# Kernel tuning notes

Hardware: AMD Instinct MI355X
Metric: run time of the kernel (lower is better)

Reference implementation:

```python
import jax, jax.numpy as jnp
import numpy as np

MARGIN = 0.35
EPS = 1e-12  # matches F.normalize default eps


def setup_inputs() -> dict:
    key = jax.random.key(0)
    k1, k2 = jax.random.split(key)
    B, N, D = 64, 1024, 128
    embeddings = jax.random.normal(k1, (B, N, D), dtype=jnp.float32)
    labels = jax.random.randint(k2, (B, N), 0, 2, dtype=jnp.int64)
    return {"embeddings": embeddings, "labels": labels}


def reference(embeddings, labels):
    # L2-normalize along last dim (F.normalize semantics)
    norm = jnp.linalg.norm(embeddings, axis=-1, keepdims=True)
    emb = embeddings / jnp.maximum(norm, EPS)  # [B, N, D]

    pos = (labels == 1)  # [B, N]
    neg = (labels == 0)  # [B, N]
    n_pos = pos.sum(axis=-1)  # [B]
    n_neg = neg.sum(axis=-1)  # [B]
    valid = (n_pos > 0) & (n_neg > 0)  # [B]

    # pairwise similarity: positive i vs negative j within each sample
    sim = jnp.einsum('bnd,bmd->bnm', emb, emb)  # [B, N, N]
    hinge = jax.nn.relu(sim - 0.5 + MARGIN)  # [B, N, N]

    # per-positive mean over negatives
    neg_f = neg.astype(emb.dtype)
    per_pos_sum = jnp.einsum('bnm,bm->bn', hinge, neg_f)  # sum over negatives
    denom = jnp.maximum(n_neg, 1).astype(emb.dtype)[:, None]
    per_pos_mean = per_pos_sum / denom  # [B, N]

    pos_f = pos.astype(emb.dtype)
    valid_f = valid.astype(emb.dtype)
    loss_sum = jnp.sum(per_pos_mean * pos_f * valid_f[:, None])
    count = jnp.sum(n_pos * valid)
    return loss_sum / jnp.maximum(count, 1).astype(emb.dtype)
```

## Files before the change

### kernel.cpp

```cpp
#include <hip/hip_runtime.h>
#include <stdint.h>


#define B_    64
#define N_    1024
#define D_    128
#define NPAD  640
#define T_    5

typedef __attribute__((ext_vector_type(8))) short short8;
typedef __attribute__((ext_vector_type(4))) float floatx4;
typedef __attribute__((ext_vector_type(4))) unsigned short ushortx4;

__device__ __forceinline__ unsigned short f2bf_rne(float f) {
    union { float f; unsigned u; } cv; cv.f = f;
    unsigned u = cv.u;
    return (unsigned short)((u + 0x7FFFu + ((u >> 16) & 1u)) >> 16);
}

__global__ __launch_bounds__(256) void scan_kernel(
    const long long* __restrict__ lab,
    unsigned short* __restrict__ posIdx,
    unsigned short* __restrict__ negIdx,
    int* __restrict__ npos)
{
    __shared__ int wsum[4];
    const int b = blockIdx.x, t = threadIdx.x;
    const int w = t >> 6, lane = t & 63;
    const long long* lb = lab + (size_t)b * N_;

    int l[4], c = 0;
    #pragma unroll
    for (int i = 0; i < 4; ++i) { l[i] = (int)lb[t * 4 + i]; c += l[i]; }

    int sc = c;
    #pragma unroll
    for (int off = 1; off < 64; off <<= 1) {
        int v = __shfl_up(sc, off);
        if (lane >= off) sc += v;
    }
    if (lane == 63) wsum[w] = sc;
    __syncthreads();
    int base = 0;
    for (int k = 0; k < w; ++k) base += wsum[k];

    int pe = base + sc - c;
    #pragma unroll
    for (int i = 0; i < 4; ++i) {
        const int n = t * 4 + i;
        if (l[i]) { if (pe < NPAD) posIdx[b * NPAD + pe] = (unsigned short)n; }
        else      { const int ne = n - pe; if (ne < NPAD) negIdx[b * NPAD + ne] = (unsigned short)n; }
        pe += l[i];
    }
    if (t == 255) npos[b] = base + sc;
}

__global__ __launch_bounds__(256) void prep_kernel(
    const float* __restrict__ emb,
    const unsigned short* __restrict__ posIdx,
    const unsigned short* __restrict__ negIdx,
    const int* __restrict__ npos,
    ushortx4* __restrict__ Apos_c,
    ushortx4* __restrict__ Aneg_c)
{
    const int w    = threadIdx.x >> 6;
    const int lane = threadIdx.x & 63;
    const int gw   = blockIdx.x * 4 + w;
    const int half = lane >> 5, sl = lane & 31;

    const int side = gw >= (B_ * NPAD / 2);
    const int p2   = side ? gw - (B_ * NPAD / 2) : gw;
    const int b    = p2 / (NPAD / 2);
    const int slot = (p2 % (NPAD / 2)) * 2 + half;

    const int np    = npos[b];
    const int count = side ? (N_ - np) : np;
    const unsigned short* idxArr = side ? negIdx : posIdx;

    float4 v = make_float4(0.f, 0.f, 0.f, 0.f);
    if (slot < count) {
        const int n = idxArr[b * NPAD + slot];
        v = *(const float4*)(emb + ((size_t)(b * N_ + n)) * D_ + sl * 4);
    }
    float ss = v.x * v.x + v.y * v.y + v.z * v.z + v.w * v.w;
    #pragma unroll
    for (int off = 16; off; off >>= 1) ss += __shfl_xor(ss, off);
    const float scale = 1.0f / fmaxf(sqrtf(ss), 1e-12f);

    ushortx4 o;
    o.x = f2bf_rne(v.x * scale); o.y = f2bf_rne(v.y * scale);
    o.z = f2bf_rne(v.z * scale); o.w = f2bf_rne(v.w * scale);
    ushortx4* dst = side ? Aneg_c : Apos_c;
    dst[(size_t)(b * NPAD + slot) * (D_ / 4) + sl] = o;
}

__global__ __launch_bounds__(256, 2) void gemm_hinge_kernel(
    const unsigned short* __restrict__ Apos_c,
    const unsigned short* __restrict__ Aneg_c,
    float* __restrict__ Stile)
{
    __shared__ unsigned short ldsA[128 * 128];
    __shared__ unsigned short ldsB[128 * 128];
    __shared__ float sred[4];

    const int t    = threadIdx.x;
    const int w    = t >> 6;
    const int lane = t & 63;
    const int tm = blockIdx.x, tn = blockIdx.y, b = blockIdx.z;

    const char* gA = (const char*)(Apos_c + ((size_t)b * NPAD + (size_t)tm * 128) * D_);
    const char* gB = (const char*)(Aneg_c + ((size_t)b * NPAD + (size_t)tn * 128) * D_);

    auto lA = (__attribute__((address_space(3))) char*)ldsA;
    auto lB = (__attribute__((address_space(3))) char*)ldsB;

    #pragma unroll
    for (int it = 0; it < 8; ++it) {
        const int p   = it * 4096 + t * 16;
        const int row = p >> 8;
        const int c   = (p >> 4) & 15;
        const int goff = (row << 8) | ((c ^ (row & 15)) << 4);
        __builtin_amdgcn_global_load_lds(
            (const __attribute__((address_space(1))) void*)(gA + goff),
            (__attribute__((address_space(3))) void*)(lA + it * 4096 + w * 1024),
            16, 0, 0);
        __builtin_amdgcn_global_load_lds(
            (const __attribute__((address_space(1))) void*)(gB + goff),
            (__attribute__((address_space(3))) void*)(lB + it * 4096 + w * 1024),
            16, 0, 0);
    }
    __syncthreads();

    const int wm = w & 1, wn = w >> 1;
    const int r = lane & 15, quad = lane >> 4;

    floatx4 acc[4][4] = {};
    #pragma unroll
    for (int ks = 0; ks < 4; ++ks) {
        short8 af[4], bf[4];
        const int cc = (((ks << 2) + quad) ^ r) << 3;
        #pragma unroll
        for (int i = 0; i < 4; ++i) {
            af[i] = *(const short8*)(ldsA + (wm * 64 + i * 16 + r) * 128 + cc);
            bf[i] = *(const short8*)(ldsB + (wn * 64 + i * 16 + r) * 128 + cc);
        }
        #pragma unroll
        for (int i = 0; i < 4; ++i)
            #pragma unroll
            for (int j = 0; j < 4; ++j)
                acc[i][j] = __builtin_amdgcn_mfma_f32_16x16x32_bf16(
                    af[i], bf[j], acc[i][j], 0, 0, 0);
    }

    float s = 0.f;
    #pragma unroll
    for (int i = 0; i < 4; ++i)
        #pragma unroll
        for (int j = 0; j < 4; ++j)
            #pragma unroll
            for (int k2 = 0; k2 < 4; ++k2)
                s += fmaxf(acc[i][j][k2] - 0.15f, 0.f);

    #pragma unroll
    for (int off = 32; off; off >>= 1) s += __shfl_down(s, off);
    if (lane == 0) sred[w] = s;
    __syncthreads();
    if (t == 0)
        Stile[b * (T_ * T_) + tm * T_ + tn] = sred[0] + sred[1] + sred[2] + sred[3];
}

__global__ void finalize_kernel(const float* __restrict__ Stile,
                                const int* __restrict__ npos,
                                float* __restrict__ out)
{
    const int b = threadIdx.x;
    const int np = npos[b];
    const int nn = N_ - np;
    float S = 0.f;
    #pragma unroll
    for (int k = 0; k < T_ * T_; ++k) S += Stile[b * (T_ * T_) + k];
    const bool valid = (np > 0) && (nn > 0);
    float ls = valid ? S / (float)nn : 0.f;
    float c  = valid ? (float)np : 0.f;
    #pragma unroll
    for (int off = 32; off; off >>= 1) {
        ls += __shfl_down(ls, off);
        c  += __shfl_down(c, off);
    }
    if (b == 0) out[0] = ls / fmaxf(c, 1.f);
}

extern "C" void kernel_launch(void* const* d_in, const int* in_sizes, int n_in,
                              void* d_out, int out_size, void* d_ws, size_t ws_size,
                              hipStream_t stream)
{
    const float*     emb = (const float*)d_in[0];
    const long long* lab = (const long long*)d_in[1];
    float* out = (float*)d_out;

    char* ws = (char*)d_ws;
    float* Stile = (float*)ws;
    int*   npos  = (int*)(ws + (16 << 10));
    unsigned short* posIdx = (unsigned short*)(ws + (32 << 10));
    unsigned short* negIdx = (unsigned short*)(ws + (160 << 10));
    unsigned short* Apos_c = (unsigned short*)(ws + (1 << 20));
    unsigned short* Aneg_c = Apos_c + (size_t)B_ * NPAD * D_;

    scan_kernel<<<B_, 256, 0, stream>>>(lab, posIdx, negIdx, npos);

    prep_kernel<<<B_ * NPAD / 4, 256, 0, stream>>>(
        emb, posIdx, negIdx, npos, (ushortx4*)Apos_c, (ushortx4*)Aneg_c);

    dim3 grid(T_, T_, B_);
    gemm_hinge_kernel<<<grid, 256, 0, stream>>>(Apos_c, Aneg_c, Stile);

    finalize_kernel<<<1, 64, 0, stream>>>(Stile, npos, out);
}
```

Measured before the change: 99.16 us.

## Use FP8 MFMA, skip empty tiles, and fuse finalize into GEMM via last-block ticket

Normalized embeddings are now packed to FP8 instead of BF16, and the GEMM uses the fp8 16x16x32 MFMA with a halved LDS footprint and an adjusted swizzle. Tiles that fall entirely in padding are skipped. The separate finalize kernel is removed: the last block, detected with an atomic ticket counter, performs the final reduction. FP8 precision raises the risk of accuracy drift in the hinge sum, and the atomic counter adds some serialization.

```diff
diff --git a/kernel.cpp b/kernel.cpp
--- a/kernel.cpp
+++ b/kernel.cpp
@@ -7,26 +7,23 @@
 #define D_    128
 #define NPAD  640
 #define T_    5
-
-typedef __attribute__((ext_vector_type(8))) short short8;
+#define NTILE (T_ * T_)
+#define NBLK  (T_ * T_ * B_)
+
 typedef __attribute__((ext_vector_type(4))) float floatx4;
 typedef __attribute__((ext_vector_type(4))) unsigned short ushortx4;
-
-__device__ __forceinline__ unsigned short f2bf_rne(float f) {
-    union { float f; unsigned u; } cv; cv.f = f;
-    unsigned u = cv.u;
-    return (unsigned short)((u + 0x7FFFu + ((u >> 16) & 1u)) >> 16);
-}
 
 __global__ __launch_bounds__(256) void scan_kernel(
     const long long* __restrict__ lab,
     unsigned short* __restrict__ posIdx,
     unsigned short* __restrict__ negIdx,
-    int* __restrict__ npos)
+    int* __restrict__ npos,
+    int* __restrict__ counter)
 {
     __shared__ int wsum[4];
     const int b = blockIdx.x, t = threadIdx.x;
     const int w = t >> 6, lane = t & 63;
+    if (b == 0 && t == 0) *counter = 0;
     const long long* lb = lab + (size_t)b * N_;
 
     int l[4], c = 0;
@@ -60,8 +57,8 @@
     const unsigned short* __restrict__ posIdx,
     const unsigned short* __restrict__ negIdx,
     const int* __restrict__ npos,
-    ushortx4* __restrict__ Apos_c,
-    ushortx4* __restrict__ Aneg_c)
+    unsigned int* __restrict__ Apos_c,
+    unsigned int* __restrict__ Aneg_c)
 {
     const int w    = threadIdx.x >> 6;
     const int lane = threadIdx.x & 63;
@@ -87,107 +84,125 @@
     for (int off = 16; off; off >>= 1) ss += __shfl_xor(ss, off);
     const float scale = 1.0f / fmaxf(sqrtf(ss), 1e-12f);
 
-    ushortx4 o;
-    o.x = f2bf_rne(v.x * scale); o.y = f2bf_rne(v.y * scale);
-    o.z = f2bf_rne(v.z * scale); o.w = f2bf_rne(v.w * scale);
-    ushortx4* dst = side ? Aneg_c : Apos_c;
-    dst[(size_t)(b * NPAD + slot) * (D_ / 4) + sl] = o;
-}
-
-__global__ __launch_bounds__(256, 2) void gemm_hinge_kernel(
-    const unsigned short* __restrict__ Apos_c,
-    const unsigned short* __restrict__ Aneg_c,
-    float* __restrict__ Stile)
-{
-    __shared__ unsigned short ldsA[128 * 128];
-    __shared__ unsigned short ldsB[128 * 128];
+    unsigned int pk = 0;
+    pk = __builtin_amdgcn_cvt_pk_fp8_f32(v.x * scale, v.y * scale, pk, false);
+    pk = __builtin_amdgcn_cvt_pk_fp8_f32(v.z * scale, v.w * scale, pk, true);
+
+    unsigned int* dst = side ? Aneg_c : Apos_c;
+    dst[(size_t)(b * NPAD + slot) * (D_ / 4) + sl] = pk;
+}
+
+__global__ __launch_bounds__(256, 3) void gemm_hinge_kernel(
+    const unsigned char* __restrict__ Apos_c,
+    const unsigned char* __restrict__ Aneg_c,
+    const int* __restrict__ npos,
+    float* __restrict__ Stile,
+    int* __restrict__ counter,
+    float* __restrict__ out)
+{
+    __shared__ unsigned char ldsA[128 * 128];
+    __shared__ unsigned char ldsB[128 * 128];
     __shared__ float sred[4];
+    __shared__ int lastFlag;
 
     const int t    = threadIdx.x;
     const int w    = t >> 6;
     const int lane = t & 63;
     const int tm = blockIdx.x, tn = blockIdx.y, b = blockIdx.z;
 
-    const char* gA = (const char*)(Apos_c + ((size_t)b * NPAD + (size_t)tm * 128) * D_);
-    const char* gB = (const char*)(Aneg_c + ((size_t)b * NPAD + (size_t)tn * 128) * D_);
-
-    auto lA = (__attribute__((address_space(3))) char*)ldsA;
-    auto lB = (__attribute__((address_space(3))) char*)ldsB;
-
-    #pragma unroll
-    for (int it = 0; it < 8; ++it) {
-        const int p   = it * 4096 + t * 16;
-        const int row = p >> 8;
-        const int c   = (p >> 4) & 15;
-        const int goff = (row << 8) | ((c ^ (row & 15)) << 4);
-        __builtin_amdgcn_global_load_lds(
-            (const __attribute__((address_space(1))) void*)(gA + goff),
-            (__attribute__((address_space(3))) void*)(lA + it * 4096 + w * 1024),
-            16, 0, 0);
-        __builtin_amdgcn_global_load_lds(
-            (const __attribute__((address_space(1))) void*)(gB + goff),
-            (__attribute__((address_space(3))) void*)(lB + it * 4096 + w * 1024),
-            16, 0, 0);
-    }
-    __syncthreads();
-
-    const int wm = w & 1, wn = w >> 1;
-    const int r = lane & 15, quad = lane >> 4;
-
-    floatx4 acc[4][4] = {};
-    #pragma unroll
-    for (int ks = 0; ks < 4; ++ks) {
-        short8 af[4], bf[4];
-        const int cc = (((ks << 2) + quad) ^ r) << 3;
-        #pragma unroll
-        for (int i = 0; i < 4; ++i) {
-            af[i] = *(const short8*)(ldsA + (wm * 64 + i * 16 + r) * 128 + cc);
-            bf[i] = *(const short8*)(ldsB + (wn * 64 + i * 16 + r) * 128 + cc);
+    const int np = npos[b];
+    const int nn = N_ - np;
+    const bool active = (tm * 128 < np) && (tn * 128 < nn);
+
+    float tileSum = 0.f;
+    if (active) {
+        const char* gA = (const char*)(Apos_c + ((size_t)b * NPAD + (size_t)tm * 128) * D_);
+        const char* gB = (const char*)(Aneg_c + ((size_t)b * NPAD + (size_t)tn * 128) * D_);
+        auto lA = (__attribute__((address_space(3))) char*)ldsA;
+        auto lB = (__attribute__((address_space(3))) char*)ldsB;
+
+        #pragma unroll
+        for (int it = 0; it < 4; ++it) {
+            const int p   = it * 4096 + t * 16;
+            const int row = p >> 7;
+            const int c   = (p >> 4) & 7;
+            const int goff = (row << 7) | ((c ^ (row & 7)) << 4);
+            __builtin_amdgcn_global_load_lds(
+                (const __attribute__((address_space(1))) void*)(gA + goff),
+                (__attribute__((address_space(3))) void*)(lA + it * 4096 + w * 1024),
+                16, 0, 0);
+            __builtin_amdgcn_global_load_lds(
+                (const __attribute__((address_space(1))) void*)(gB + goff),
+                (__attribute__((address_space(3))) void*)(lB + it * 4096 + w * 1024),
+                16, 0, 0);
         }
+        __syncthreads();
+
+        const int wm = w & 1, wn = w >> 1;
+        const int r = lane & 15, quad = lane >> 4;
+        const int rx = r & 7;
+
+        floatx4 acc[4][4] = {};
+        #pragma unroll
+        for (int ks = 0; ks < 4; ++ks) {
+            long af[4], bf[4];
+            const int boff = (((ks * 2 + (quad >> 1)) ^ rx) << 4) + (quad & 1) * 8;
+            #pragma unroll
+            for (int i = 0; i < 4; ++i) {
+                af[i] = *(const long*)(ldsA + (wm * 64 + i * 16 + r) * 128 + boff);
+                bf[i] = *(const long*)(ldsB + (wn * 64 + i * 16 + r) * 128 + boff);
+            }
+            #pragma unroll
+            for (int i = 0; i < 4; ++i)
+                #pragma unroll
+                for (int j = 0; j < 4; ++j)
+                    acc[i][j] = __builtin_amdgcn_mfma_f32_16x16x32_fp8_fp8(
+                        af[i], bf[j], acc[i][j], 0, 0, 0);
+        }
+
+        float s = 0.f;
         #pragma unroll
         for (int i = 0; i < 4; ++i)
             #pragma unroll
             for (int j = 0; j < 4; ++j)
-                acc[i][j] = __builtin_amdgcn_mfma_f32_16x16x32_bf16(
-                    af[i], bf[j], acc[i][j], 0, 0, 0);
-    }
-
-    float s = 0.f;
-    #pragma unroll
-    for (int i = 0; i < 4; ++i)
-        #pragma unroll
-        for (int j = 0; j < 4; ++j)
-            #pragma unroll
-            for (int k2 = 0; k2 < 4; ++k2)
-                s += fmaxf(acc[i][j][k2] - 0.15f, 0.f);
-
-    #pragma unroll
-    for (int off = 32; off; off >>= 1) s += __shfl_down(s, off);
-    if (lane == 0) sred[w] = s;
+                #pragma unroll
+                for (int k2 = 0; k2 < 4; ++k2)
+                    s += fmaxf(acc[i][j][k2] - 0.15f, 0.f);
+
+        #pragma unroll
+        for (int off = 32; off; off >>= 1) s += __shfl_down(s, off);
+        if (lane == 0) sred[w] = s;
+        __syncthreads();
+        tileSum = sred[0] + sred[1] + sred[2] + sred[3];
+    }
+
+    if (t == 0) {
+        atomicExch(&Stile[b * NTILE + tm * T_ + tn], tileSum);
+        __threadfence();
+        const int ticket = atomicAdd(counter, 1);
+        lastFlag = (ticket == NBLK - 1);
+    }
     __syncthreads();
-    if (t == 0)
-        Stile[b * (T_ * T_) + tm * T_ + tn] = sred[0] + sred[1] + sred[2] + sred[3];
-}
-
-__global__ void finalize_kernel(const float* __restrict__ Stile,
-                                const int* __restrict__ npos,
-                                float* __restrict__ out)
-{
-    const int b = threadIdx.x;
-    const int np = npos[b];
-    const int nn = N_ - np;
-    float S = 0.f;
-    #pragma unroll
-    for (int k = 0; k < T_ * T_; ++k) S += Stile[b * (T_ * T_) + k];
-    const bool valid = (np > 0) && (nn > 0);
-    float ls = valid ? S / (float)nn : 0.f;
-    float c  = valid ? (float)np : 0.f;
-    #pragma unroll
-    for (int off = 32; off; off >>= 1) {
-        ls += __shfl_down(ls, off);
-        c  += __shfl_down(c, off);
-    }
-    if (b == 0) out[0] = ls / fmaxf(c, 1.f);
+
+    if (lastFlag && t < 64) {
+        __threadfence();
+        const int bb = t;
+        float S = 0.f;
+        #pragma unroll
+        for (int k = 0; k < NTILE; ++k)
+            S += atomicAdd(&Stile[bb * NTILE + k], 0.f);
+        const int np2 = npos[bb];
+        const int nn2 = N_ - np2;
+        const bool valid = (np2 > 0) && (nn2 > 0);
+        float ls = valid ? S / (float)max(nn2, 1) : 0.f;
+        float c  = valid ? (float)np2 : 0.f;
+        #pragma unroll
+        for (int off = 32; off; off >>= 1) {
+            ls += __shfl_down(ls, off);
+            c  += __shfl_down(c, off);
+        }
+        if (t == 0) out[0] = ls / fmaxf(c, 1.f);
+    }
 }
 
 extern "C" void kernel_launch(void* const* d_in, const int* in_sizes, int n_in,
@@ -201,18 +216,19 @@
     char* ws = (char*)d_ws;
     float* Stile = (float*)ws;
     int*   npos  = (int*)(ws + (16 << 10));
+    int*   counter = (int*)(ws + (20 << 10));
     unsigned short* posIdx = (unsigned short*)(ws + (32 << 10));
     unsigned short* negIdx = (unsigned short*)(ws + (160 << 10));
-    unsigned short* Apos_c = (unsigned short*)(ws + (1 << 20));
-    unsigned short* Aneg_c = Apos_c + (size_t)B_ * NPAD * D_;
-
-    scan_kernel<<<B_, 256, 0, stream>>>(lab, posIdx, negIdx, npos);
+    unsigned int* Apos_c = (unsigned int*)(ws + (1 << 20));
+    unsigned int* Aneg_c = Apos_c + (size_t)B_ * NPAD * (D_ / 4);
+
+    scan_kernel<<<B_, 256, 0, stream>>>(lab, posIdx, negIdx, npos, counter);
 
     prep_kernel<<<B_ * NPAD / 4, 256, 0, stream>>>(
-        emb, posIdx, negIdx, npos, (ushortx4*)Apos_c, (ushortx4*)Aneg_c);
+        emb, posIdx, negIdx, npos, Apos_c, Aneg_c);
 
     dim3 grid(T_, T_, B_);
-    gemm_hinge_kernel<<<grid, 256, 0, stream>>>(Apos_c, Aneg_c, Stile);
-
-    finalize_kernel<<<1, 64, 0, stream>>>(Stile, npos, out);
-}
+    gemm_hinge_kernel<<<grid, 256, 0, stream>>>(
+        (const unsigned char*)Apos_c, (const unsigned char*)Aneg_c,
+        npos, Stile, counter, out);
+}
```

Measured after the change: 135.4 us. 36.5% more time.
